# Optimization experiments

Measured on AMD Instinct MI355X. Metric: run time of the kernel, lower is better.

## Reference

```python
import jax, jax.numpy as jnp
import numpy as np

NODE_NUM = 2000
BN_EPS = 1e-5


def _gin_conv(x, W, b, src, dst, n):
    # h = Linear(x); out = relu(scatter_add_j h_j + (1+eps)*h_i), eps=0
    h = x @ W.T + b
    agg = jax.ops.segment_sum(h[src], dst, num_segments=n)
    return jax.nn.relu(agg + h)


def _batchnorm(x, g, b):
    mu = x.mean(0)
    var = x.var(0)
    return g * (x - mu) * jax.lax.rsqrt(var + BN_EPS) + b


def _leaky(x):
    return jnp.where(x >= 0, x, 0.1 * x)


def setup_inputs() -> dict:
    key = jax.random.key(0)
    ks = jax.random.split(key, 12)
    N, E = 32000, 512000
    D_IN, D_H, D_E, C = 256, 512, 256, 2
    x = jax.random.normal(ks[0], (N, D_IN), dtype=jnp.float32)
    edge_index = jax.random.randint(ks[1], (2, E), 0, N, dtype=jnp.int64)
    def lin(k, fout, fin):
        bound = 1.0 / np.sqrt(fin)
        k1, k2 = jax.random.split(k)
        W = jax.random.uniform(k1, (fout, fin), minval=-bound, maxval=bound, dtype=jnp.float32)
        b = jax.random.uniform(k2, (fout,), minval=-bound, maxval=bound, dtype=jnp.float32)
        return W, b
    W1, b1 = lin(ks[2], D_H, D_IN)
    W2, b2 = lin(ks[3], D_H, D_H)
    W3, b3 = lin(ks[4], D_E, D_H)
    Wp, bp = lin(ks[5], C, D_E)
    return {
        "x": x, "edge_index": edge_index,
        "W1": W1, "b1": b1, "W2": W2, "b2": b2, "W3": W3, "b3": b3,
        "g1": jnp.ones((D_H,), jnp.float32), "be1": jnp.zeros((D_H,), jnp.float32),
        "g2": jnp.ones((D_H,), jnp.float32), "be2": jnp.zeros((D_H,), jnp.float32),
        "g3": jnp.ones((D_E,), jnp.float32), "be3": jnp.zeros((D_E,), jnp.float32),
        "Wp": Wp, "bp": bp,
    }


def reference(x, edge_index, W1, b1, W2, b2, W3, b3, g1, be1, g2, be2, g3, be3, Wp, bp):
    n = x.shape[0]
    src, dst = edge_index[0], edge_index[1]
    h = _gin_conv(x, W1, b1, src, dst, n)
    h = _leaky(_batchnorm(h, g1, be1))
    h = _gin_conv(h, W2, b2, src, dst, n)
    h = _leaky(_batchnorm(h, g2, be2))
    h = _gin_conv(h, W3, b3, src, dst, n)
    h = _leaky(_batchnorm(h, g3, be3))
    emb = h.shape[-1]
    h = h.reshape(-1, NODE_NUM, emb)
    # PowerMeanAggregation with learned p initialized to 1.0 -> mean over nodes
    g = h.mean(axis=1)  # [B, emb]
    output = g @ Wp.T + bp  # [B, num_class]
    ypred = jnp.argmax(output, axis=1)
    return output, ypred
```

## Files before the change

### kernel.cpp

```cpp
#include <hip/hip_runtime.h>

#define N_NODES 32000
typedef unsigned short u16;
typedef unsigned int u32;
typedef unsigned char u8;
typedef __attribute__((ext_vector_type(8))) short bf16x8;
typedef __attribute__((ext_vector_type(4))) float f32x4;
typedef __attribute__((ext_vector_type(2))) float f32x2;

__device__ __forceinline__ float leakyf(float v) { return v >= 0.f ? v : 0.1f * v; }
__device__ __forceinline__ u16 f2bf(float f) {
    u32 u = __float_as_uint(f);
    return (u16)((u + 0x7FFFu + ((u >> 16) & 1u)) >> 16);
}
__device__ __forceinline__ float bf_lo(u32 u) { return __uint_as_float(u << 16); }
__device__ __forceinline__ float bf_hi(u32 u) { return __uint_as_float(u & 0xFFFF0000u); }
__device__ __forceinline__ u32 pack2(float a, float b) { return (u32)f2bf(a) | ((u32)f2bf(b) << 16); }

__device__ __forceinline__ void dec4(float* acc, u32 w) {
    f32x2 lo = __builtin_amdgcn_cvt_pk_f32_fp8(w, false);
    f32x2 hi = __builtin_amdgcn_cvt_pk_f32_fp8(w, true);
    acc[0] += lo[0]; acc[1] += lo[1]; acc[2] += hi[0]; acc[3] += hi[1];
}
__device__ __forceinline__ void dec16(float* acc, uint4 v) {
    dec4(acc + 0, v.x); dec4(acc + 4, v.y); dec4(acc + 8, v.z); dec4(acc + 12, v.w);
}
__device__ __forceinline__ u8 f2fp8(float v) {
    return (u8)__builtin_amdgcn_cvt_pk_fp8_f32(v, v, 0, false);
}

__device__ __forceinline__ void gload16(const u16* g, u16* l) {
    __builtin_amdgcn_global_load_lds((const __attribute__((address_space(1))) void*)g,
                                     (__attribute__((address_space(3))) void*)l, 16, 0, 0);
}

__global__ __launch_bounds__(256) void k_prep(const int* __restrict__ dst, int* __restrict__ cnt, int E,
                                              const float* __restrict__ x, u32* __restrict__ x8,
                                              const float* __restrict__ W1, const float* __restrict__ W2,
                                              const float* __restrict__ W3, u16* __restrict__ o1,
                                              u16* __restrict__ o2, u16* __restrict__ o3)
{
    const int b = blockIdx.x, t = threadIdx.x;
    if (b < 2000) {
        int e = b * 256 + t;
        if (e < E) atomicAdd(&cnt[dst[e]], 1);
    } else if (b < 10000) {
        int i = (b - 2000) * 256 + t;
        float4 v = ((const float4*)x)[i];
        int p = __builtin_amdgcn_cvt_pk_fp8_f32(v.x, v.y, 0, false);
        p = __builtin_amdgcn_cvt_pk_fp8_f32(v.z, v.w, p, true);
        x8[i] = (u32)p;
    } else {
        int bb = b - 10000;
        const float* in; u16* out; int i;
        if (bb < 128)      { in = W1; out = o1; i = bb * 256 + t; }
        else if (bb < 384) { in = W2; out = o2; i = (bb - 128) * 256 + t; }
        else               { in = W3; out = o3; i = (bb - 384) * 256 + t; }
        float4 v = ((const float4*)in)[i];
        ushort4 o;
        o.x = f2bf(v.x); o.y = f2bf(v.y); o.z = f2bf(v.z); o.w = f2bf(v.w);
        ((ushort4*)out)[i] = o;
    }
}

__global__ __launch_bounds__(256) void k_scan_blk(const int* __restrict__ cnt, int* __restrict__ rp,
                                                  int* __restrict__ bsum)
{
    __shared__ int sh[256];
    const int b = blockIdx.x, t = threadIdx.x;
    int v = cnt[b * 256 + t];
    sh[t] = v;
    __syncthreads();
    for (int off = 1; off < 256; off <<= 1) {
        int u = (t >= off) ? sh[t - off] : 0;
        __syncthreads();
        sh[t] += u;
        __syncthreads();
    }
    rp[b * 256 + t] = sh[t] - v;
    if (t == 255) bsum[b] = sh[255];
}

__global__ __launch_bounds__(256) void k_scan_add(int* __restrict__ rp, const int* __restrict__ bsum,
                                                  int nb, int n, int E)
{
    __shared__ int sh[256];
    const int b = blockIdx.x, t = threadIdx.x;
    int v = (t < b && t < nb) ? bsum[t] : 0;
    sh[t] = v;
    __syncthreads();
    for (int off = 128; off > 0; off >>= 1) {
        if (t < off) sh[t] += sh[t + off];
        __syncthreads();
    }
    int i = b * 256 + t;
    rp[i] += sh[0];
    if (i == 0) rp[n] = E;
}

__global__ __launch_bounds__(256) void k_place(const int* __restrict__ src, const int* __restrict__ dst,
                                               const int* __restrict__ rp, int* __restrict__ cur,
                                               int* __restrict__ cs, int E)
{
    int e = blockIdx.x * 256 + threadIdx.x;
    if (e < E) {
        int d = dst[e];
        int p = rp[d] + atomicAdd(&cur[d], 1);
        cs[p] = src[e];
    }
}

template <bool RELU, bool DEGB, bool F8OUT, bool STATS>
__global__ __launch_bounds__(256) void k_gemm_mfma(const u16* __restrict__ A, const u16* __restrict__ W,
                                                   const float* __restrict__ bias, const int* __restrict__ rp,
                                                   void* __restrict__ Cv, float* __restrict__ partial,
                                                   int K, int OD)
{
    __shared__ u16 As[2][128 * 32];
    __shared__ u16 Bs[2][128 * 32];
    const int t = threadIdx.x;
    const int lane = t & 63;
    const int w = t >> 6;
    const int wr = w >> 1, wc = w & 1;
    const int bm = blockIdx.x * 128;
    const int bn = blockIdx.y * 128;

    const int c0 = w * 64 + lane;
    const int r0 = c0 >> 2, kc0 = (c0 & 3) * 8;
    const int c1 = c0 + 256;
    const int r1 = c1 >> 2, kc1 = (c1 & 3) * 8;
    const u16* gA0 = A + (size_t)(bm + r0) * K + kc0;
    const u16* gA1 = A + (size_t)(bm + r1) * K + kc1;
    const u16* gB0 = W + (size_t)(bn + r0) * K + kc0;
    const u16* gB1 = W + (size_t)(bn + r1) * K + kc1;

    f32x4 acc[4][4];
#pragma unroll
    for (int i = 0; i < 4; ++i)
#pragma unroll
        for (int j = 0; j < 4; ++j)
            acc[i][j] = (f32x4){0.f, 0.f, 0.f, 0.f};

    const int fr = lane & 15;
    const int ko = (lane >> 4) * 8;

    auto STAGE = [&](int b, int k0) {
        gload16(gA0 + k0, &As[b][0] + w * 512);
        gload16(gA1 + k0, &As[b][0] + 2048 + w * 512);
        gload16(gB0 + k0, &Bs[b][0] + w * 512);
        gload16(gB1 + k0, &Bs[b][0] + 2048 + w * 512);
    };

    STAGE(0, 0);

    int cur = 0;
    for (int k0 = 0; k0 < K; k0 += 32) {
        if (k0 + 32 < K) {
            STAGE(cur ^ 1, k0 + 32);
            asm volatile("s_waitcnt vmcnt(4)" ::: "memory");
        } else {
            asm volatile("s_waitcnt vmcnt(0)" ::: "memory");
        }
        __syncthreads();
        bf16x8 af[4], bfv[4];
#pragma unroll
        for (int i = 0; i < 4; ++i)
            af[i] = *(const bf16x8*)&As[cur][(wr * 64 + i * 16 + fr) * 32 + ko];
#pragma unroll
        for (int j = 0; j < 4; ++j)
            bfv[j] = *(const bf16x8*)&Bs[cur][(wc * 64 + j * 16 + fr) * 32 + ko];
#pragma unroll
        for (int i = 0; i < 4; ++i)
#pragma unroll
            for (int j = 0; j < 4; ++j)
                acc[i][j] = __builtin_amdgcn_mfma_f32_16x16x32_bf16(af[i], bfv[j], acc[i][j], 0, 0, 0);
        __syncthreads();
        cur ^= 1;
    }

    u16* C16 = (u16*)Cv;
    u8*  C8  = (u8*)Cv;
    const int qr = (lane >> 4) * 4;
    float bcol[4];
#pragma unroll
    for (int j = 0; j < 4; ++j) bcol[j] = bias[bn + wc * 64 + j * 16 + fr];
    float s4[4] = {}, q4[4] = {};
#pragma unroll
    for (int i = 0; i < 4; ++i) {
#pragma unroll
        for (int r = 0; r < 4; ++r) {
            int row = bm + wr * 64 + i * 16 + qr + r;
            float bm_ = 1.f;
            if (DEGB) bm_ = (float)(rp[row + 1] - rp[row]) + 1.f;
#pragma unroll
            for (int j = 0; j < 4; ++j) {
                int col = bn + wc * 64 + j * 16 + fr;
                float o = acc[i][j][r] + bm_ * bcol[j];
                if (RELU) o = fmaxf(o, 0.f);
                if (STATS) { s4[j] += o; q4[j] = fmaf(o, o, q4[j]); }
                if (F8OUT) C8[(size_t)row * OD + col] = f2fp8(o);
                else       C16[(size_t)row * OD + col] = f2bf(o);
            }
        }
    }

    if (STATS) {
#pragma unroll
        for (int j = 0; j < 4; ++j) {
            s4[j] += __shfl_xor(s4[j], 16); s4[j] += __shfl_xor(s4[j], 32);
            q4[j] += __shfl_xor(q4[j], 16); q4[j] += __shfl_xor(q4[j], 32);
        }
        __syncthreads();
        float* sred = (float*)&As[0][0];
        if ((lane >> 4) == 0) {
#pragma unroll
            for (int j = 0; j < 4; ++j) {
                sred[((w * 4 + j) * 16 + fr) * 2 + 0] = s4[j];
                sred[((w * 4 + j) * 16 + fr) * 2 + 1] = q4[j];
            }
        }
        __syncthreads();
        if (wr == 0 && (lane >> 4) == 0) {
#pragma unroll
            for (int j = 0; j < 4; ++j) {
                int i0 = ((w * 4 + j) * 16 + fr) * 2;
                int i1 = (((w + 2) * 4 + j) * 16 + fr) * 2;
                float ss = sred[i0] + sred[i1];
                float qq = sred[i0 + 1] + sred[i1 + 1];
                int col = bn + wc * 64 + j * 16 + fr;
                partial[(size_t)blockIdx.x * 1024 + col]       = ss;
                partial[(size_t)blockIdx.x * 1024 + 512 + col] = qq;
            }
        }
    }
}

template <bool RELU>
__global__ __launch_bounds__(256) void k_agg256_f8(const u8* __restrict__ h8, const int* __restrict__ rp,
                                                   const int* __restrict__ cs, u16* __restrict__ out)
{
    const int lane = threadIdx.x & 63;
    const int n = blockIdx.x * 4 + (threadIdx.x >> 6);
    const int g = lane >> 4;
    const int c = lane & 15;
    const uint4* hb = (const uint4*)h8 + c;

    float acc[16];
#pragma unroll
    for (int i = 0; i < 16; ++i) acc[i] = 0.f;
    if (g == 0) dec16(acc, hb[(size_t)n * 16]);

    const int beg = rp[n], end = rp[n + 1];
    int e = beg;
    for (; e + 16 <= end; e += 16) {
        uint4 v0 = hb[(size_t)cs[e + g] * 16];
        uint4 v1 = hb[(size_t)cs[e + 4 + g] * 16];
        uint4 v2 = hb[(size_t)cs[e + 8 + g] * 16];
        uint4 v3 = hb[(size_t)cs[e + 12 + g] * 16];
        dec16(acc, v0); dec16(acc, v1); dec16(acc, v2); dec16(acc, v3);
    }
    for (; e + 4 <= end; e += 4) {
        uint4 v = hb[(size_t)cs[e + g] * 16];
        dec16(acc, v);
    }
    if (e + g < end) {
        uint4 v = hb[(size_t)cs[e + g] * 16];
        dec16(acc, v);
    }
#pragma unroll
    for (int i = 0; i < 16; ++i) acc[i] += __shfl_xor(acc[i], 16);
#pragma unroll
    for (int i = 0; i < 16; ++i) acc[i] += __shfl_xor(acc[i], 32);
    if (g == 0) {
        if (RELU) {
#pragma unroll
            for (int i = 0; i < 16; ++i) acc[i] = fmaxf(acc[i], 0.f);
        }
        uint4 o0, o1;
        o0.x = pack2(acc[0], acc[1]);  o0.y = pack2(acc[2], acc[3]);
        o0.z = pack2(acc[4], acc[5]);  o0.w = pack2(acc[6], acc[7]);
        o1.x = pack2(acc[8], acc[9]);  o1.y = pack2(acc[10], acc[11]);
        o1.z = pack2(acc[12], acc[13]); o1.w = pack2(acc[14], acc[15]);
        uint4* op = (uint4*)((u32*)out + (size_t)n * 128 + c * 8);
        op[0] = o0; op[1] = o1;
    }
}

template <bool RELU>
__global__ __launch_bounds__(256) void k_agg512_f8(const u8* __restrict__ h8, const int* __restrict__ rp,
                                                   const int* __restrict__ cs, u16* __restrict__ out)
{
    const int lane = threadIdx.x & 63;
    const int n = blockIdx.x * 4 + (threadIdx.x >> 6);
    const int g = lane >> 5;
    const int c = lane & 31;
    const uint4* hb = (const uint4*)h8 + c;

    float acc[16];
#pragma unroll
    for (int i = 0; i < 16; ++i) acc[i] = 0.f;
    if (g == 0) dec16(acc, hb[(size_t)n * 32]);

    const int beg = rp[n], end = rp[n + 1];
    int e = beg;
    for (; e + 8 <= end; e += 8) {
        uint4 v0 = hb[(size_t)cs[e + g] * 32];
        uint4 v1 = hb[(size_t)cs[e + 2 + g] * 32];
        uint4 v2 = hb[(size_t)cs[e + 4 + g] * 32];
        uint4 v3 = hb[(size_t)cs[e + 6 + g] * 32];
        dec16(acc, v0); dec16(acc, v1); dec16(acc, v2); dec16(acc, v3);
    }
    for (; e + 2 <= end; e += 2) {
        uint4 v = hb[(size_t)cs[e + g] * 32];
        dec16(acc, v);
    }
    if (e + g < end) {
        uint4 v = hb[(size_t)cs[e + g] * 32];
        dec16(acc, v);
    }
#pragma unroll
    for (int i = 0; i < 16; ++i) acc[i] += __shfl_xor(acc[i], 32);
    if (g == 0) {
        if (RELU) {
#pragma unroll
            for (int i = 0; i < 16; ++i) acc[i] = fmaxf(acc[i], 0.f);
        }
        uint4 o0, o1;
        o0.x = pack2(acc[0], acc[1]);  o0.y = pack2(acc[2], acc[3]);
        o0.z = pack2(acc[4], acc[5]);  o0.w = pack2(acc[6], acc[7]);
        o1.x = pack2(acc[8], acc[9]);  o1.y = pack2(acc[10], acc[11]);
        o1.z = pack2(acc[12], acc[13]); o1.w = pack2(acc[14], acc[15]);
        uint4* op = (uint4*)((u32*)out + (size_t)n * 256 + c * 8);
        op[0] = o0; op[1] = o1;
    }
}

template <int D>
__global__ __launch_bounds__(256) void k_bn_part(const u16* __restrict__ h, float* __restrict__ partial)
{
    constexpr int SLOT = D / 8;
    constexpr int NS = 256 / SLOT;
    constexpr int ROWS = 16;
    const int t = threadIdx.x;
    const int s = t % SLOT, j = t / SLOT;
    const int r0 = blockIdx.x * ROWS;
    float a[8] = {}, q[8] = {};
#pragma unroll
    for (int rr = 0; rr < ROWS / NS; ++rr) {
        int r = j + rr * NS;
        uint4 v = *((const uint4*)(h + (size_t)(r0 + r) * D) + s);
        u32 wv[4] = {v.x, v.y, v.z, v.w};
#pragma unroll
        for (int k = 0; k < 4; ++k) {
            float lo = bf_lo(wv[k]), hi = bf_hi(wv[k]);
            a[2 * k]     += lo; q[2 * k]     = fmaf(lo, lo, q[2 * k]);
            a[2 * k + 1] += hi; q[2 * k + 1] = fmaf(hi, hi, q[2 * k + 1]);
        }
    }
    __shared__ float red[16][256];
#pragma unroll
    for (int i = 0; i < 8; ++i) { red[i][t] = a[i]; red[8 + i][t] = q[i]; }
    __syncthreads();
    if (j == 0) {
        for (int k = 1; k < NS; ++k) {
            int o = k * SLOT + s;
#pragma unroll
            for (int i = 0; i < 8; ++i) { a[i] += red[i][o]; q[i] += red[8 + i][o]; }
        }
        float* pb = partial + (size_t)blockIdx.x * (2 * D);
        float4* p0 = (float4*)(pb + 8 * s);
        p0[0] = make_float4(a[0], a[1], a[2], a[3]);
        p0[1] = make_float4(a[4], a[5], a[6], a[7]);
        float4* p1 = (float4*)(pb + D + 8 * s);
        p1[0] = make_float4(q[0], q[1], q[2], q[3]);
        p1[1] = make_float4(q[4], q[5], q[6], q[7]);
    }
}

template <int D, int P, int SEG>
__global__ __launch_bounds__(256) void k_bn_red1(const float* __restrict__ partial, float* __restrict__ part2)
{
    const int g = blockIdx.x * 256 + threadIdx.x;
    const int col = g & (2 * D - 1);
    const int seg = g / (2 * D);
    constexpr int CHUNK = P / SEG;
    const float* p = partial + (size_t)seg * CHUNK * (2 * D) + col;
    float acc = 0.f;
#pragma unroll
    for (int i = 0; i < CHUNK; ++i) acc += p[(size_t)i * (2 * D)];
    part2[(size_t)seg * (2 * D) + col] = acc;
}

template <int D, int SEG>
__global__ __launch_bounds__(256) void k_bn_red2(const float* __restrict__ part2, float* __restrict__ sums)
{
    const int col = blockIdx.x * 256 + threadIdx.x;
    float acc = 0.f;
#pragma unroll
    for (int i = 0; i < SEG; ++i) acc += part2[(size_t)i * (2 * D) + col];
    sums[col] = acc;
}

template <int D>
__global__ __launch_bounds__(256) void k_bn_apply(u16* __restrict__ h, const float* __restrict__ sums,
                                                  const float* __restrict__ gam, const float* __restrict__ bet)
{
    int i = blockIdx.x * 256 + threadIdx.x;
    int c = (i * 8) & (D - 1);
    const float invN = 1.f / (float)N_NODES;
    float sc[8], sh[8];
#pragma unroll
    for (int k = 0; k < 8; ++k) {
        float mu  = sums[c + k] * invN;
        float var = sums[D + c + k] * invN - mu * mu;
        float rs  = rsqrtf(var + 1e-5f);
        sc[k] = gam[c + k] * rs;
        sh[k] = bet[c + k] - mu * sc[k];
    }
    uint4 v = ((uint4*)h)[i];
    u32 vv[4] = {v.x, v.y, v.z, v.w};
    u32 r[4];
#pragma unroll
    for (int k = 0; k < 4; ++k) {
        float a = leakyf(fmaf(bf_lo(vv[k]), sc[2 * k], sh[2 * k]));
        float b = leakyf(fmaf(bf_hi(vv[k]), sc[2 * k + 1], sh[2 * k + 1]));
        r[k] = pack2(a, b);
    }
    ((uint4*)h)[i] = make_uint4(r[0], r[1], r[2], r[3]);
}

__global__ __launch_bounds__(256) void k_pool_bn(const u16* __restrict__ h, const float* __restrict__ sums,
                                                 const float* __restrict__ gam, const float* __restrict__ bet,
                                                 float* __restrict__ ppool)
{
    const int t = threadIdx.x;
    const int s = t & 31;
    const int j = t >> 5;
    const int r0 = blockIdx.x * 16;
    const float invN = 1.f / (float)N_NODES;
    float sc[8], sh[8];
#pragma unroll
    for (int k = 0; k < 8; ++k) {
        int c = 8 * s + k;
        float mu  = sums[c] * invN;
        float var = sums[256 + c] * invN - mu * mu;
        float rs  = rsqrtf(var + 1e-5f);
        sc[k] = gam[c] * rs;
        sh[k] = bet[c] - mu * sc[k];
    }
    float a[8] = {};
#pragma unroll
    for (int rr = 0; rr < 2; ++rr) {
        int r = r0 + j + rr * 8;
        uint4 v = *((const uint4*)(h + (size_t)r * 256) + s);
        u32 wv[4] = {v.x, v.y, v.z, v.w};
#pragma unroll
        for (int k = 0; k < 4; ++k) {
            a[2 * k]     += leakyf(fmaf(bf_lo(wv[k]), sc[2 * k], sh[2 * k]));
            a[2 * k + 1] += leakyf(fmaf(bf_hi(wv[k]), sc[2 * k + 1], sh[2 * k + 1]));
        }
    }
    __shared__ float red[8][256];
#pragma unroll
    for (int i = 0; i < 8; ++i) red[i][t] = a[i];
    __syncthreads();
    if (j == 0) {
#pragma unroll
        for (int k = 1; k < 8; ++k) {
            int o = k * 32 + s;
#pragma unroll
            for (int i = 0; i < 8; ++i) a[i] += red[i][o];
        }
        float4* pb = (float4*)(ppool + (size_t)blockIdx.x * 256 + 8 * s);
        pb[0] = make_float4(a[0], a[1], a[2], a[3]);
        pb[1] = make_float4(a[4], a[5], a[6], a[7]);
    }
}

__global__ __launch_bounds__(256) void k_head(const float* __restrict__ ppool, const float* __restrict__ Wp,
                                              const float* __restrict__ bp, float* __restrict__ out)
{
    __shared__ float r0s[256], r1s[256];
    const int b = blockIdx.x, t = threadIdx.x;
    const float* p = ppool + (size_t)b * 125 * 256 + t;
    float g = 0.f;
#pragma unroll 5
    for (int i = 0; i < 125; ++i) g += p[(size_t)i * 256];
    g *= (1.f / 2000.f);
    r0s[t] = g * Wp[t];
    r1s[t] = g * Wp[256 + t];
    __syncthreads();
    for (int off = 128; off > 0; off >>= 1) {
        if (t < off) { r0s[t] += r0s[t + off]; r1s[t] += r1s[t + off]; }
        __syncthreads();
    }
    if (t == 0) {
        float o0 = r0s[0] + bp[0];
        float o1 = r1s[0] + bp[1];
        out[b * 2]     = o0;
        out[b * 2 + 1] = o1;
        out[32 + b]    = (o1 > o0) ? 1.f : 0.f;
    }
}

extern "C" void kernel_launch(void* const* d_in, const int* in_sizes, int n_in,
                              void* d_out, int out_size, void* d_ws, size_t ws_size,
                              hipStream_t stream)
{
    const float* x   = (const float*)d_in[0];
    const int*   ei  = (const int*)d_in[1];
    const float* W1  = (const float*)d_in[2];
    const float* b1  = (const float*)d_in[3];
    const float* W2  = (const float*)d_in[4];
    const float* b2  = (const float*)d_in[5];
    const float* W3  = (const float*)d_in[6];
    const float* b3  = (const float*)d_in[7];
    const float* g1  = (const float*)d_in[8];
    const float* be1 = (const float*)d_in[9];
    const float* g2  = (const float*)d_in[10];
    const float* be2 = (const float*)d_in[11];
    const float* g3  = (const float*)d_in[12];
    const float* be3 = (const float*)d_in[13];
    const float* Wp  = (const float*)d_in[14];
    const float* bp  = (const float*)d_in[15];
    float* out = (float*)d_out;

    const int E = in_sizes[1] / 2;
    const int* src = ei;
    const int* dst = ei + E;

    char* ws = (char*)d_ws;
    size_t off = 0;
    auto alloc = [&](size_t bytes) -> void* {
        void* p = ws + off;
        off = (off + bytes + 255) & ~(size_t)255;
        return p;
    };
    u16*   bufA = (u16*)alloc((size_t)N_NODES * 512 * 2);
    u16*   bufB = (u16*)alloc((size_t)N_NODES * 512 * 2);
    u8*    buf8 = (u8*)alloc((size_t)N_NODES * 512);
    u8*    x8   = (u8*)alloc((size_t)N_NODES * 256);
    u16*   w1b  = (u16*)alloc(512 * 256 * 2);
    u16*   w2b  = (u16*)alloc(512 * 512 * 2);
    u16*   w3b  = (u16*)alloc(256 * 512 * 2);
    int*   cs   = (int*)alloc((size_t)E * 4);
    int*   rp   = (int*)alloc((size_t)(N_NODES + 1) * 4);
    int*   cnt  = (int*)alloc((size_t)N_NODES * 4 * 2);
    int*   cur  = cnt + N_NODES;
    const size_t zbytes = (size_t)N_NODES * 8;
    int*   bsum = (int*)alloc(256 * 4);
    float* part = (float*)alloc((size_t)2000 * 1024 * 4);
    float* part2 = (float*)alloc((size_t)100 * 1024 * 4);
    float* sums1 = (float*)alloc(1024 * 4);
    float* sums2 = (float*)alloc(1024 * 4);
    float* sums3 = (float*)alloc(1024 * 4);
    float* ppool = (float*)alloc((size_t)2000 * 256 * 4);

    hipMemsetAsync(cnt, 0, zbytes, stream);

    const int eb = (E + 255) / 256;
    const int nb = N_NODES / 256;

    k_prep<<<eb + 8000 + 512, 256, 0, stream>>>(dst, cnt, E, x, (u32*)x8, W1, W2, W3, w1b, w2b, w3b);
    k_scan_blk<<<nb, 256, 0, stream>>>(cnt, rp, bsum);
    k_scan_add<<<nb, 256, 0, stream>>>(rp, bsum, nb, N_NODES, E);
    k_place<<<eb, 256, 0, stream>>>(src, dst, rp, cur, cs, E);

    const int PB = N_NODES / 16;

    k_agg256_f8<false><<<N_NODES / 4, 256, 0, stream>>>(x8, rp, cs, bufA);
    k_gemm_mfma<true, true, false, true><<<dim3(250, 4), 256, 0, stream>>>(bufA, w1b, b1, rp, bufB, part, 256, 512);
    k_bn_red1<512, 250, 25><<<100, 256, 0, stream>>>(part, part2);
    k_bn_red2<512, 25><<<4, 256, 0, stream>>>(part2, sums1);
    k_bn_apply<512><<<N_NODES * 512 / 8 / 256, 256, 0, stream>>>(bufB, sums1, g1, be1);

    k_gemm_mfma<false, false, true, false><<<dim3(250, 4), 256, 0, stream>>>(bufB, w2b, b2, rp, buf8, nullptr, 512, 512);
    k_agg512_f8<true><<<N_NODES / 4, 256, 0, stream>>>(buf8, rp, cs, bufA);
    k_bn_part<512><<<PB, 256, 0, stream>>>(bufA, part);
    k_bn_red1<512, 2000, 100><<<400, 256, 0, stream>>>(part, part2);
    k_bn_red2<512, 100><<<4, 256, 0, stream>>>(part2, sums2);
    k_bn_apply<512><<<N_NODES * 512 / 8 / 256, 256, 0, stream>>>(bufA, sums2, g2, be2);

    k_gemm_mfma<false, false, true, false><<<dim3(250, 2), 256, 0, stream>>>(bufA, w3b, b3, rp, buf8, nullptr, 512, 256);
    k_agg256_f8<true><<<N_NODES / 4, 256, 0, stream>>>(buf8, rp, cs, bufB);
    k_bn_part<256><<<PB, 256, 0, stream>>>(bufB, part);
    k_bn_red1<256, 2000, 100><<<200, 256, 0, stream>>>(part, part2);
    k_bn_red2<256, 100><<<2, 256, 0, stream>>>(part2, sums3);

    k_pool_bn<<<PB, 256, 0, stream>>>(bufB, sums3, g3, be3, ppool);
    k_head<<<16, 256, 0, stream>>>(ppool, Wp, bp, out);
}
```

Baseline: 323.7 us.

## Fuse batchnorm partial statistics into layer 2 and 3 aggregation kernels

Replaces the separate k_bn_part passes with aggregation kernels that accumulate per-column sum and sum of squares in shared memory while producing each node's output. Each block now handles 16 nodes (4 per wave) and writes per-block partials in the same layout the downstream reduction expects. This removes a full re-read of the bf16 activation buffer and one launch per layer. In exchange, the grid is four times smaller, and the stats are taken from fp32 values before bf16 rounding, which differs slightly from reading back the stored activations.

```diff
diff --git a/kernel.cpp b/kernel.cpp
--- a/kernel.cpp
+++ b/kernel.cpp
@@ -286,94 +286,141 @@
     }
 }
 
-template <bool RELU>
-__global__ __launch_bounds__(256) void k_agg512_f8(const u8* __restrict__ h8, const int* __restrict__ rp,
-                                                   const int* __restrict__ cs, u16* __restrict__ out)
-{
-    const int lane = threadIdx.x & 63;
-    const int n = blockIdx.x * 4 + (threadIdx.x >> 6);
+__global__ __launch_bounds__(256) void k_agg512_f8s(const u8* __restrict__ h8, const int* __restrict__ rp,
+                                                    const int* __restrict__ cs, u16* __restrict__ out,
+                                                    float* __restrict__ partial)
+{
+    __shared__ float sw[4][1024];
+    const int t = threadIdx.x;
+    const int w = t >> 6;
+    const int lane = t & 63;
     const int g = lane >> 5;
     const int c = lane & 31;
+    for (int i = lane; i < 1024; i += 64) sw[w][i] = 0.f;
     const uint4* hb = (const uint4*)h8 + c;
 
-    float acc[16];
-#pragma unroll
-    for (int i = 0; i < 16; ++i) acc[i] = 0.f;
-    if (g == 0) dec16(acc, hb[(size_t)n * 32]);
-
-    const int beg = rp[n], end = rp[n + 1];
-    int e = beg;
-    for (; e + 8 <= end; e += 8) {
-        uint4 v0 = hb[(size_t)cs[e + g] * 32];
-        uint4 v1 = hb[(size_t)cs[e + 2 + g] * 32];
-        uint4 v2 = hb[(size_t)cs[e + 4 + g] * 32];
-        uint4 v3 = hb[(size_t)cs[e + 6 + g] * 32];
-        dec16(acc, v0); dec16(acc, v1); dec16(acc, v2); dec16(acc, v3);
-    }
-    for (; e + 2 <= end; e += 2) {
-        uint4 v = hb[(size_t)cs[e + g] * 32];
-        dec16(acc, v);
-    }
-    if (e + g < end) {
-        uint4 v = hb[(size_t)cs[e + g] * 32];
-        dec16(acc, v);
-    }
-#pragma unroll
-    for (int i = 0; i < 16; ++i) acc[i] += __shfl_xor(acc[i], 32);
-    if (g == 0) {
-        if (RELU) {
-#pragma unroll
-            for (int i = 0; i < 16; ++i) acc[i] = fmaxf(acc[i], 0.f);
-        }
-        uint4 o0, o1;
-        o0.x = pack2(acc[0], acc[1]);  o0.y = pack2(acc[2], acc[3]);
-        o0.z = pack2(acc[4], acc[5]);  o0.w = pack2(acc[6], acc[7]);
-        o1.x = pack2(acc[8], acc[9]);  o1.y = pack2(acc[10], acc[11]);
-        o1.z = pack2(acc[12], acc[13]); o1.w = pack2(acc[14], acc[15]);
-        uint4* op = (uint4*)((u32*)out + (size_t)n * 256 + c * 8);
-        op[0] = o0; op[1] = o1;
-    }
-}
-
-template <int D>
-__global__ __launch_bounds__(256) void k_bn_part(const u16* __restrict__ h, float* __restrict__ partial)
-{
-    constexpr int SLOT = D / 8;
-    constexpr int NS = 256 / SLOT;
-    constexpr int ROWS = 16;
+#pragma unroll 1
+    for (int nn = 0; nn < 4; ++nn) {
+        const int n = blockIdx.x * 16 + w * 4 + nn;
+        float acc[16];
+#pragma unroll
+        for (int i = 0; i < 16; ++i) acc[i] = 0.f;
+        if (g == 0) dec16(acc, hb[(size_t)n * 32]);
+        const int beg = rp[n], end = rp[n + 1];
+        int e = beg;
+        for (; e + 8 <= end; e += 8) {
+            uint4 v0 = hb[(size_t)cs[e + g] * 32];
+            uint4 v1 = hb[(size_t)cs[e + 2 + g] * 32];
+            uint4 v2 = hb[(size_t)cs[e + 4 + g] * 32];
+            uint4 v3 = hb[(size_t)cs[e + 6 + g] * 32];
+            dec16(acc, v0); dec16(acc, v1); dec16(acc, v2); dec16(acc, v3);
+        }
+        for (; e + 2 <= end; e += 2) {
+            uint4 v = hb[(size_t)cs[e + g] * 32];
+            dec16(acc, v);
+        }
+        if (e + g < end) {
+            uint4 v = hb[(size_t)cs[e + g] * 32];
+            dec16(acc, v);
+        }
+#pragma unroll
+        for (int i = 0; i < 16; ++i) acc[i] += __shfl_xor(acc[i], 32);
+        if (g == 0) {
+#pragma unroll
+            for (int i = 0; i < 16; ++i) {
+                float a = fmaxf(acc[i], 0.f);
+                acc[i] = a;
+                sw[w][i * 32 + c] += a;
+                sw[w][512 + i * 32 + c] = fmaf(a, a, sw[w][512 + i * 32 + c]);
+            }
+            uint4 o0, o1;
+            o0.x = pack2(acc[0], acc[1]);  o0.y = pack2(acc[2], acc[3]);
+            o0.z = pack2(acc[4], acc[5]);  o0.w = pack2(acc[6], acc[7]);
+            o1.x = pack2(acc[8], acc[9]);  o1.y = pack2(acc[10], acc[11]);
+            o1.z = pack2(acc[12], acc[13]); o1.w = pack2(acc[14], acc[15]);
+            uint4* op = (uint4*)((u32*)out + (size_t)n * 256 + c * 8);
+            op[0] = o0; op[1] = o1;
+        }
+    }
+    __syncthreads();
+    float* pb = partial + (size_t)blockIdx.x * 1024;
+#pragma unroll
+    for (int r = 0; r < 4; ++r) {
+        int o = t + r * 256;
+        int base = (o < 512) ? 0 : 512;
+        int col = o - base;
+        int addr = base + (col & 15) * 32 + (col >> 4);
+        pb[o] = sw[0][addr] + sw[1][addr] + sw[2][addr] + sw[3][addr];
+    }
+}
+
+__global__ __launch_bounds__(256) void k_agg256_f8s(const u8* __restrict__ h8, const int* __restrict__ rp,
+                                                    const int* __restrict__ cs, u16* __restrict__ out,
+                                                    float* __restrict__ partial)
+{
+    __shared__ float sw[4][512];
     const int t = threadIdx.x;
-    const int s = t % SLOT, j = t / SLOT;
-    const int r0 = blockIdx.x * ROWS;
-    float a[8] = {}, q[8] = {};
-#pragma unroll
-    for (int rr = 0; rr < ROWS / NS; ++rr) {
-        int r = j + rr * NS;
-        uint4 v = *((const uint4*)(h + (size_t)(r0 + r) * D) + s);
-        u32 wv[4] = {v.x, v.y, v.z, v.w};
-#pragma unroll
-        for (int k = 0; k < 4; ++k) {
-            float lo = bf_lo(wv[k]), hi = bf_hi(wv[k]);
-            a[2 * k]     += lo; q[2 * k]     = fmaf(lo, lo, q[2 * k]);
-            a[2 * k + 1] += hi; q[2 * k + 1] = fmaf(hi, hi, q[2 * k + 1]);
-        }
-    }
-    __shared__ float red[16][256];
-#pragma unroll
-    for (int i = 0; i < 8; ++i) { red[i][t] = a[i]; red[8 + i][t] = q[i]; }
+    const int w = t >> 6;
+    const int lane = t & 63;
+    const int g = lane >> 4;
+    const int c = lane & 15;
+    for (int i = lane; i < 512; i += 64) sw[w][i] = 0.f;
+    const uint4* hb = (const uint4*)h8 + c;
+
+#pragma unroll 1
+    for (int nn = 0; nn < 4; ++nn) {
+        const int n = blockIdx.x * 16 + w * 4 + nn;
+        float acc[16];
+#pragma unroll
+        for (int i = 0; i < 16; ++i) acc[i] = 0.f;
+        if (g == 0) dec16(acc, hb[(size_t)n * 16]);
+        const int beg = rp[n], end = rp[n + 1];
+        int e = beg;
+        for (; e + 16 <= end; e += 16) {
+            uint4 v0 = hb[(size_t)cs[e + g] * 16];
+            uint4 v1 = hb[(size_t)cs[e + 4 + g] * 16];
+            uint4 v2 = hb[(size_t)cs[e + 8 + g] * 16];
+            uint4 v3 = hb[(size_t)cs[e + 12 + g] * 16];
+            dec16(acc, v0); dec16(acc, v1); dec16(acc, v2); dec16(acc, v3);
+        }
+        for (; e + 4 <= end; e += 4) {
+            uint4 v = hb[(size_t)cs[e + g] * 16];
+            dec16(acc, v);
+        }
+        if (e + g < end) {
+            uint4 v = hb[(size_t)cs[e + g] * 16];
+            dec16(acc, v);
+        }
+#pragma unroll
+        for (int i = 0; i < 16; ++i) acc[i] += __shfl_xor(acc[i], 16);
+#pragma unroll
+        for (int i = 0; i < 16; ++i) acc[i] += __shfl_xor(acc[i], 32);
+        if (g == 0) {
+#pragma unroll
+            for (int i = 0; i < 16; ++i) {
+                float a = fmaxf(acc[i], 0.f);
+                acc[i] = a;
+                sw[w][i * 16 + c] += a;
+                sw[w][256 + i * 16 + c] = fmaf(a, a, sw[w][256 + i * 16 + c]);
+            }
+            uint4 o0, o1;
+            o0.x = pack2(acc[0], acc[1]);  o0.y = pack2(acc[2], acc[3]);
+            o0.z = pack2(acc[4], acc[5]);  o0.w = pack2(acc[6], acc[7]);
+            o1.x = pack2(acc[8], acc[9]);  o1.y = pack2(acc[10], acc[11]);
+            o1.z = pack2(acc[12], acc[13]); o1.w = pack2(acc[14], acc[15]);
+            uint4* op = (uint4*)((u32*)out + (size_t)n * 128 + c * 8);
+            op[0] = o0; op[1] = o1;
+        }
+    }
     __syncthreads();
-    if (j == 0) {
-        for (int k = 1; k < NS; ++k) {
-            int o = k * SLOT + s;
-#pragma unroll
-            for (int i = 0; i < 8; ++i) { a[i] += red[i][o]; q[i] += red[8 + i][o]; }
-        }
-        float* pb = partial + (size_t)blockIdx.x * (2 * D);
-        float4* p0 = (float4*)(pb + 8 * s);
-        p0[0] = make_float4(a[0], a[1], a[2], a[3]);
-        p0[1] = make_float4(a[4], a[5], a[6], a[7]);
-        float4* p1 = (float4*)(pb + D + 8 * s);
-        p1[0] = make_float4(q[0], q[1], q[2], q[3]);
-        p1[1] = make_float4(q[4], q[5], q[6], q[7]);
+    float* pb = partial + (size_t)blockIdx.x * 512;
+#pragma unroll
+    for (int r = 0; r < 2; ++r) {
+        int o = t + r * 256;
+        int base = (o < 256) ? 0 : 256;
+        int col = o - base;
+        int addr = base + (col & 15) * 16 + (col >> 4);
+        pb[o] = sw[0][addr] + sw[1][addr] + sw[2][addr] + sw[3][addr];
     }
 }
 
@@ -566,8 +613,6 @@
     k_scan_add<<<nb, 256, 0, stream>>>(rp, bsum, nb, N_NODES, E);
     k_place<<<eb, 256, 0, stream>>>(src, dst, rp, cur, cs, E);
 
-    const int PB = N_NODES / 16;
-
     k_agg256_f8<false><<<N_NODES / 4, 256, 0, stream>>>(x8, rp, cs, bufA);
     k_gemm_mfma<true, true, false, true><<<dim3(250, 4), 256, 0, stream>>>(bufA, w1b, b1, rp, bufB, part, 256, 512);
     k_bn_red1<512, 250, 25><<<100, 256, 0, stream>>>(part, part2);
@@ -575,18 +620,16 @@
     k_bn_apply<512><<<N_NODES * 512 / 8 / 256, 256, 0, stream>>>(bufB, sums1, g1, be1);
 
     k_gemm_mfma<false, false, true, false><<<dim3(250, 4), 256, 0, stream>>>(bufB, w2b, b2, rp, buf8, nullptr, 512, 512);
-    k_agg512_f8<true><<<N_NODES / 4, 256, 0, stream>>>(buf8, rp, cs, bufA);
-    k_bn_part<512><<<PB, 256, 0, stream>>>(bufA, part);
+    k_agg512_f8s<<<N_NODES / 16, 256, 0, stream>>>(buf8, rp, cs, bufA, part);
     k_bn_red1<512, 2000, 100><<<400, 256, 0, stream>>>(part, part2);
     k_bn_red2<512, 100><<<4, 256, 0, stream>>>(part2, sums2);
     k_bn_apply<512><<<N_NODES * 512 / 8 / 256, 256, 0, stream>>>(bufA, sums2, g2, be2);
 
     k_gemm_mfma<false, false, true, false><<<dim3(250, 2), 256, 0, stream>>>(bufA, w3b, b3, rp, buf8, nullptr, 512, 256);
-    k_agg256_f8<true><<<N_NODES / 4, 256, 0, stream>>>(buf8, rp, cs, bufB);
-    k_bn_part<256><<<PB, 256, 0, stream>>>(bufB, part);
+    k_agg256_f8s<<<N_NODES / 16, 256, 0, stream>>>(buf8, rp, cs, bufB, part);
     k_bn_red1<256, 2000, 100><<<200, 256, 0, stream>>>(part, part2);
     k_bn_red2<256, 100><<<2, 256, 0, stream>>>(part2, sums3);
 
-    k_pool_bn<<<PB, 256, 0, stream>>>(bufB, sums3, g3, be3, ppool);
+    k_pool_bn<<<N_NODES / 16, 256, 0, stream>>>(bufB, sums3, g3, be3, ppool);
     k_head<<<16, 256, 0, stream>>>(ppool, Wp, bp, out);
 }
```

Result: slower. 333.9 us (+3.1%).
